# Kernel tuning notes

Hardware: AMD Instinct MI355X
Metric: run time of the kernel (lower is better)

Reference implementation:

```python
import jax, jax.numpy as jnp
import numpy as np

HEADS = 8
DIM_HEAD = 64
SCALE = DIM_HEAD ** -0.5

def layernorm_ch(x, g, eps=1e-5):
    # channel-wise LayerNorm over dim=1 (NCHW), biased variance
    mean = jnp.mean(x, axis=1, keepdims=True)
    var = jnp.var(x, axis=1, keepdims=True)
    return (x - mean) * jax.lax.rsqrt(var + eps) * g[None, :, None, None]

def setup_inputs() -> dict:
    key = jax.random.key(0)
    ks = jax.random.split(key, 4)
    B, C, H, W = 16, 512, 64, 64
    hidden = HEADS * DIM_HEAD
    x = jax.random.normal(ks[0], (B, C, H, W), dtype=jnp.float32)
    w_qkv = jax.random.normal(ks[1], (3 * hidden, C), dtype=jnp.float32) * (C ** -0.5)
    w_out = jax.random.normal(ks[2], (C, hidden), dtype=jnp.float32) * (hidden ** -0.5)
    b_out = jnp.zeros((C,), dtype=jnp.float32)
    g_out = jnp.ones((C,), dtype=jnp.float32)
    g_ln = jnp.ones((C,), dtype=jnp.float32)
    return {"x": x, "w_qkv": w_qkv, "w_out": w_out, "b_out": b_out, "g_out": g_out, "g_ln": g_ln}

def reference(x, w_qkv, w_out, b_out, g_out, g_ln):
    B, C, H, W = x.shape
    n = H * W
    x_norm = layernorm_ch(x, g_ln)
    # 1x1 conv == channel GEMM: [B,3*hidden,H,W]
    qkv = jnp.einsum('oc,bchw->bohw', w_qkv, x_norm)
    q, k, v = jnp.split(qkv, 3, axis=1)
    # b (h d) x y -> b h d n
    def to_heads(t):
        return t.reshape(B, HEADS, DIM_HEAD, n)
    q, k, v = to_heads(q), to_heads(k), to_heads(v)
    q = jax.nn.softmax(q, axis=-2) * SCALE   # softmax over d
    k = jax.nn.softmax(k, axis=-1)           # softmax over n
    v = v / n
    context = jnp.einsum('bhdn,bhen->bhde', k, v)
    out = jnp.einsum('bhde,bhdn->bhen', context, q)
    out = out.reshape(B, HEADS * DIM_HEAD, H, W)
    out = jnp.einsum('oc,bchw->bohw', w_out, out) + b_out[None, :, None, None]
    out = layernorm_ch(out, g_out)
    return out + x
```

## Files before the change

### kernel.cpp

```cpp
#include <hip/hip_runtime.h>
#include <math.h>

#define CCH    512
#define HWN    4096
#define NPIX   65536
#define OC3    1536
#define QSCALE 0.125f
#define LN_EPS 1e-5f

typedef _Float16 h16;
typedef h16  f16x8 __attribute__((ext_vector_type(8)));
typedef h16  f16x4 __attribute__((ext_vector_type(4)));
typedef float f32x4 __attribute__((ext_vector_type(4)));

__device__ __forceinline__ float waveReduceSum(float v) {
#pragma unroll
    for (int off = 32; off; off >>= 1) v += __shfl_xor(v, off);
    return v;
}

__device__ __forceinline__ void gl_lds16(const void* g, void* l) {
    __builtin_amdgcn_global_load_lds((const __attribute__((address_space(1))) void*)g,
                                     (__attribute__((address_space(3))) void*)l, 16, 0, 0);
}

__global__ __launch_bounds__(256) void transpose_prep(const float* __restrict__ src,
                                                      h16* __restrict__ dhi,
                                                      float* __restrict__ psum,
                                                      float* __restrict__ psq,
                                                      const float* __restrict__ w_qkv,
                                                      const float* __restrict__ g_ln,
                                                      const float* __restrict__ w_out,
                                                      h16* __restrict__ wg_h,
                                                      float* __restrict__ s,
                                                      h16* __restrict__ wo_h) {
    __shared__ float tile[64][65];
    __shared__ float ps1[4][64], ps2[4][64];
    const int t = threadIdx.x;

    if (blockIdx.z == 16) {
        const int o = (blockIdx.x + 64 * blockIdx.y) * 4 + (t >> 6);
        const int lane = t & 63;
        if (o < OC3) {
            float sum = 0.f;
#pragma unroll
            for (int j = 0; j < 8; ++j) {
                const int c = lane + j * 64;
                const float w = w_qkv[(size_t)o * CCH + c] * g_ln[c];
                wg_h[(size_t)o * CCH + c] = (h16)(w * 64.f);
                sum += w;
            }
            sum = waveReduceSum(sum);
            if (lane == 0) s[o] = sum;
        } else {
            const int r = o - OC3;
#pragma unroll
            for (int j = 0; j < 8; ++j) {
                const int c = lane + j * 64;
                wo_h[(size_t)r * CCH + c] = (h16)(w_out[(size_t)r * CCH + c] * 64.f);
            }
        }
        return;
    }

    const int b = blockIdx.z, c0 = blockIdx.y * 64, p0 = blockIdx.x * 64;
    const float* sb = src + ((size_t)b * CCH + c0) * HWN + p0;
    const int rc = t >> 4, cc4 = (t & 15) * 4;
#pragma unroll
    for (int ps = 0; ps < 4; ++ps) {
        const float4 v = *(const float4*)(sb + (size_t)(rc + ps * 16) * HWN + cc4);
        tile[rc + ps * 16][cc4 + 0] = v.x;
        tile[rc + ps * 16][cc4 + 1] = v.y;
        tile[rc + ps * 16][cc4 + 2] = v.z;
        tile[rc + ps * 16][cc4 + 3] = v.w;
    }
    __syncthreads();
    {
        const int q = t >> 6, px = t & 63;
        float s1 = 0.f, s2 = 0.f;
#pragma unroll
        for (int c = q * 16; c < q * 16 + 16; ++c) {
            const float v = tile[c][px];
            s1 += v; s2 += v * v;
        }
        ps1[q][px] = s1; ps2[q][px] = s2;
    }
    const int pr0 = t >> 3, cs = (t & 7) * 8;
#pragma unroll
    for (int ps = 0; ps < 2; ++ps) {
        const int pr = pr0 + ps * 32;
        f16x8 vh;
#pragma unroll
        for (int q = 0; q < 8; ++q) vh[q] = (h16)tile[cs + q][pr];
        const size_t o = ((size_t)b * HWN + p0 + pr) * CCH + c0 + cs;
        *(f16x8*)(dhi + o) = vh;
    }
    __syncthreads();
    if (t < 64) {
        const float s1 = ps1[0][t] + ps1[1][t] + ps1[2][t] + ps1[3][t];
        const float s2 = ps2[0][t] + ps2[1][t] + ps2[2][t] + ps2[3][t];
        const size_t gp = (size_t)b * HWN + p0 + t;
        psum[(size_t)(c0 >> 6) * NPIX + gp] = s1;
        psq [(size_t)(c0 >> 6) * NPIX + gp] = s2;
    }
}

__global__ __launch_bounds__(512) void qkv_gemm(const h16* __restrict__ Ahg,
                                                const h16* __restrict__ Bhg,
                                                const float* __restrict__ sv,
                                                const float* __restrict__ psum,
                                                const float* __restrict__ psq,
                                                h16* __restrict__ qout) {
    __shared__ __align__(16) h16 Ah[8192];
    __shared__ __align__(16) h16 Bh[16384];
    __shared__ float mnS[256], rsS[256];
    const int tid = threadIdx.x;
    const int om = blockIdx.x * 128;
    const int by0 = blockIdx.y;
    const int by  = (by0 & 7) * 32 + (by0 >> 3);
    const int p0  = by * 256;

    const int srow = tid >> 2;
    const int skh  = ((tid & 3) ^ (srow & 3)) * 8;
    const size_t a0 = (size_t)(om + srow) * CCH + skh;
    const size_t b0 = (size_t)(p0 + srow) * CCH + skh;

    const int lane = tid & 63;
    const int wv = tid >> 6;
    const int wm = (wv >> 2) * 64, wn = (wv & 3) * 64;
    const int lr = lane & 15, kg = lane >> 4;
    const int swz = (kg ^ (lr & 3)) * 8;

    f32x4 acc[4][4];
#pragma unroll
    for (int i = 0; i < 4; ++i)
#pragma unroll
        for (int j = 0; j < 4; ++j) acc[i][j] = {0.f, 0.f, 0.f, 0.f};

#define STAGE(KC)                                                          \
    do {                                                                   \
        gl_lds16(Ahg + a0 + (KC),                 Ah + tid * 8);           \
        gl_lds16(Ahg + a0 + (KC) + 32,            Ah + 4096 + tid * 8);    \
        gl_lds16(Bhg + b0 + (KC),                 Bh + tid * 8);           \
        gl_lds16(Bhg + b0 + (KC) + 128 * CCH,     Bh + 4096 + tid * 8);    \
        gl_lds16(Bhg + b0 + (KC) + 32,            Bh + 8192 + tid * 8);    \
        gl_lds16(Bhg + b0 + (KC) + 32 + 128 * CCH, Bh + 12288 + tid * 8);  \
    } while (0)

    STAGE(0);
    if (tid < 256) {
        const int gp = p0 + tid;
        float s1 = 0.f, s2 = 0.f;
#pragma unroll
        for (int cb = 0; cb < 8; ++cb) {
            s1 += psum[(size_t)cb * NPIX + gp];
            s2 += psq [(size_t)cb * NPIX + gp];
        }
        const float m = s1 * (1.f / 512.f);
        float var = s2 * (1.f / 512.f) - m * m;
        var = fmaxf(var, 0.f);
        mnS[tid] = m;
        rsS[tid] = rsqrtf(var + LN_EPS);
    }

#pragma unroll 1
    for (int kc = 0; kc < 512; kc += 64) {
        __syncthreads();
        f16x8 a0f[4], b0f[4], a1f[4], b1f[4];
#pragma unroll
        for (int i = 0; i < 4; ++i) {
            a0f[i] = *(const f16x8*)(Ah + (wm + i * 16 + lr) * 32 + swz);
            b0f[i] = *(const f16x8*)(Bh + (wn + i * 16 + lr) * 32 + swz);
        }
#pragma unroll
        for (int i = 0; i < 4; ++i)
#pragma unroll
            for (int j = 0; j < 4; ++j)
                acc[i][j] = __builtin_amdgcn_mfma_f32_16x16x32_f16(a0f[i], b0f[j], acc[i][j], 0, 0, 0);
#pragma unroll
        for (int i = 0; i < 4; ++i) {
            a1f[i] = *(const f16x8*)(Ah + 4096 + (wm + i * 16 + lr) * 32 + swz);
            b1f[i] = *(const f16x8*)(Bh + 8192 + (wn + i * 16 + lr) * 32 + swz);
        }
        __syncthreads();
        if (kc + 64 < 512) STAGE(kc + 64);
#pragma unroll
        for (int i = 0; i < 4; ++i)
#pragma unroll
            for (int j = 0; j < 4; ++j)
                acc[i][j] = __builtin_amdgcn_mfma_f32_16x16x32_f16(a1f[i], b1f[j], acc[i][j], 0, 0, 0);
    }
#undef STAGE

    const int b = p0 >> 12, hw0 = p0 & 4095;
    float mn[4], rs[4];
#pragma unroll
    for (int j = 0; j < 4; ++j) {
        const int px = wn + j * 16 + lr;
        mn[j] = mnS[px]; rs[j] = rsS[px];
    }
#pragma unroll
    for (int i = 0; i < 4; ++i)
#pragma unroll
        for (int r = 0; r < 4; ++r) {
            const int o = om + wm + i * 16 + kg * 4 + r;
            const float so = sv[o];
            h16* dst = qout + ((size_t)b * OC3 + o) * HWN;
#pragma unroll
            for (int j = 0; j < 4; ++j) {
                const int hw = hw0 + wn + j * 16 + lr;
                dst[hw] = (h16)(rs[j] * (acc[i][j][r] * (1.f / 64.f) - mn[j] * so));
            }
        }
}

__global__ __launch_bounds__(64) void ctx_partial(const h16* __restrict__ qkv16,
                                                  float* __restrict__ ctp) {
    const int bh = blockIdx.y, ci = blockIdx.x;
    const int b = bh >> 3, h = bh & 7;
    const h16* kb = qkv16 + ((size_t)b * OC3 + CCH  + h * 64) * HWN;
    const h16* vb = qkv16 + ((size_t)b * OC3 + 1024 + h * 64) * HWN;
    const int lane = threadIdx.x;
    const int lr = lane & 15, kg = lane >> 4;
    const int nbase = ci * 256 + kg * 8;

    float m[4] = {-1e30f, -1e30f, -1e30f, -1e30f};
#pragma unroll 1
    for (int c = 0; c < 8; ++c) {
        const int n0 = nbase + c * 32;
#pragma unroll
        for (int i = 0; i < 4; ++i) {
            const f16x8 kv = *(const f16x8*)(kb + (size_t)(i * 16 + lr) * HWN + n0);
#pragma unroll
            for (int u = 0; u < 8; ++u) m[i] = fmaxf(m[i], (float)kv[u]);
        }
    }
#pragma unroll
    for (int i = 0; i < 4; ++i) {
        m[i] = fmaxf(m[i], __shfl_xor(m[i], 16));
        m[i] = fmaxf(m[i], __shfl_xor(m[i], 32));
    }

    float z[4] = {0.f, 0.f, 0.f, 0.f};
    f32x4 acc[4][4];
#pragma unroll
    for (int i = 0; i < 4; ++i)
#pragma unroll
        for (int j = 0; j < 4; ++j) acc[i][j] = {0.f, 0.f, 0.f, 0.f};

#pragma unroll 1
    for (int c = 0; c < 8; ++c) {
        const int n0 = nbase + c * 32;
        f16x8 ke[4], vf[4];
#pragma unroll
        for (int j = 0; j < 4; ++j)
            vf[j] = *(const f16x8*)(vb + (size_t)(j * 16 + lr) * HWN + n0);
#pragma unroll
        for (int i = 0; i < 4; ++i) {
            const f16x8 kv = *(const f16x8*)(kb + (size_t)(i * 16 + lr) * HWN + n0);
            f16x8 t;
#pragma unroll
            for (int u = 0; u < 8; ++u) {
                const float e = __expf((float)kv[u] - m[i]);
                z[i] += e;
                t[u] = (h16)e;
            }
            ke[i] = t;
        }
#pragma unroll
        for (int i = 0; i < 4; ++i)
#pragma unroll
            for (int j = 0; j < 4; ++j)
                acc[i][j] = __builtin_amdgcn_mfma_f32_16x16x32_f16(ke[i], vf[j], acc[i][j], 0, 0, 0);
    }
#pragma unroll
    for (int i = 0; i < 4; ++i) {
        z[i] += __shfl_xor(z[i], 16);
        z[i] += __shfl_xor(z[i], 32);
    }
    float* dst = ctp + ((size_t)bh * 16 + ci) * 4224;
#pragma unroll
    for (int i = 0; i < 4; ++i)
#pragma unroll
        for (int j = 0; j < 4; ++j)
#pragma unroll
            for (int r = 0; r < 4; ++r)
                dst[(i * 16 + kg * 4 + r) * 64 + j * 16 + lr] = acc[i][j][r];
    if (kg == 0)
#pragma unroll
        for (int i = 0; i < 4; ++i) {
            dst[4096 + i * 16 + lr] = z[i];
            dst[4160 + i * 16 + lr] = m[i];
        }
}

__global__ __launch_bounds__(256) void ctx_reduce(const float* __restrict__ ctp,
                                                  h16* __restrict__ ctt) {
    __shared__ float w[16][64];
    __shared__ float rz[64];
    const int bh = blockIdx.x;
    const int tid = threadIdx.x;
    const float* src = ctp + (size_t)bh * 16 * 4224;
    if (tid < 64) {
        float M = -1e30f;
#pragma unroll
        for (int ci = 0; ci < 16; ++ci)
            M = fmaxf(M, src[(size_t)ci * 4224 + 4160 + tid]);
        float Z = 0.f;
#pragma unroll
        for (int ci = 0; ci < 16; ++ci) {
            const float ww = __expf(src[(size_t)ci * 4224 + 4160 + tid] - M);
            w[ci][tid] = ww;
            Z += ww * src[(size_t)ci * 4224 + 4096 + tid];
        }
        rz[tid] = 1.f / Z;
    }
    __syncthreads();
    h16* dstt = ctt + (size_t)bh * 4096;
    for (int e4 = tid * 4; e4 < 4096; e4 += 1024) {
        const int d = e4 >> 6, e0 = e4 & 63;
        float4 sum = make_float4(0.f, 0.f, 0.f, 0.f);
#pragma unroll
        for (int ci = 0; ci < 16; ++ci) {
            const float4 v = *(const float4*)(src + (size_t)ci * 4224 + e4);
            const float ww = w[ci][d];
            sum.x += ww * v.x; sum.y += ww * v.y;
            sum.z += ww * v.z; sum.w += ww * v.w;
        }
        const float r = rz[d];
        dstt[(e0 + 0) * 64 + d] = (h16)(sum.x * r);
        dstt[(e0 + 1) * 64 + d] = (h16)(sum.y * r);
        dstt[(e0 + 2) * 64 + d] = (h16)(sum.z * r);
        dstt[(e0 + 3) * 64 + d] = (h16)(sum.w * r);
    }
}

__global__ __launch_bounds__(512) void out_fused(const h16* __restrict__ wo_hi,
                                                 const h16* __restrict__ qkv16,
                                                 const h16* __restrict__ ctt,
                                                 const float* __restrict__ b_out,
                                                 const float* __restrict__ g_out,
                                                 const float* __restrict__ x,
                                                 float* __restrict__ out) {
    __shared__ __align__(16) h16 Alds[512 * 32];
    __shared__ __align__(16) h16 qt[128][72];
    __shared__ float red1[4][128], red2[4][128];
    __shared__ float mnS[128], rsS[128];

    const int tid = threadIdx.x;
    const int p0 = blockIdx.x * 128;
    const int b = p0 >> 12, hw0 = p0 & 4095;

    const int trow = tid >> 2;
    const int skh  = ((tid & 3) ^ (trow & 3)) * 8;
    const size_t aoff = (size_t)trow * CCH + skh;
    const int wofs = (tid >> 6) * 512;

    const int wv = tid >> 6;
    const int lane = tid & 63;
    const int lr = lane & 15, kg = lane >> 4;
    const int wm = (wv >> 1) * 128, wn = (wv & 1) * 64;
    const int swz = (kg ^ (lr & 3)) * 8;
    const int pv_e0 = (wv & 3) * 16, pv_ph = (wv >> 2) * 64;
    const int sm_px = tid >> 2, sm_d0 = (tid & 3) * 16;
    const int ql_d = tid >> 3, ql_px = (tid & 7) * 16;

    f32x4 acc[8][4];
#pragma unroll
    for (int i = 0; i < 8; ++i)
#pragma unroll
        for (int j = 0; j < 4; ++j) acc[i][j] = {0.f, 0.f, 0.f, 0.f};

#define STAGEF(S)                                                           \
    do {                                                                    \
        const int kc_ = (S) * 32;                                           \
        gl_lds16(wo_hi + aoff + kc_,               Alds + wofs);            \
        gl_lds16(wo_hi + aoff + kc_ + 128 * CCH,   Alds + 4096 + wofs);     \
        gl_lds16(wo_hi + aoff + kc_ + 256 * CCH,   Alds + 8192 + wofs);     \
        gl_lds16(wo_hi + aoff + kc_ + 384 * CCH,   Alds + 12288 + wofs);    \
    } while (0)

    STAGEF(0);

    f16x8 q0, q1;
    {
        const h16* qb = qkv16 + ((size_t)b * OC3) * HWN + hw0;
        q0 = *(const f16x8*)(qb + (size_t)ql_d * HWN + ql_px);
        q1 = *(const f16x8*)(qb + (size_t)ql_d * HWN + ql_px + 8);
    }

#pragma unroll 1
    for (int h = 0; h < 8; ++h) {
#pragma unroll
        for (int u = 0; u < 8; ++u) {
            qt[ql_px + u][ql_d]     = q0[u];
            qt[ql_px + 8 + u][ql_d] = q1[u];
        }
        __syncthreads();
        {
            float qv[16];
            float mx = -1e30f;
#pragma unroll
            for (int dd = 0; dd < 16; ++dd) {
                qv[dd] = (float)qt[sm_px][sm_d0 + dd];
                mx = fmaxf(mx, qv[dd]);
            }
            mx = fmaxf(mx, __shfl_xor(mx, 1));
            mx = fmaxf(mx, __shfl_xor(mx, 2));
            float sm = 0.f;
#pragma unroll
            for (int dd = 0; dd < 16; ++dd) {
                qv[dd] = __expf(qv[dd] - mx);
                sm += qv[dd];
            }
            sm += __shfl_xor(sm, 1);
            sm += __shfl_xor(sm, 2);
            const float sc = 512.f * QSCALE / sm;
#pragma unroll
            for (int dd = 0; dd < 16; ++dd)
                qt[sm_px][sm_d0 + dd] = (h16)(qv[dd] * sc);
        }
        __syncthreads();
        {
            const h16* cb = ctt + ((size_t)(b * 8 + h)) * 4096 + (pv_e0 + lr) * 64 + kg * 8;
            const f16x8 af0 = *(const f16x8*)(cb);
            const f16x8 af1 = *(const f16x8*)(cb + 32);
            f32x4 acc4[4];
#pragma unroll
            for (int j = 0; j < 4; ++j) acc4[j] = {0.f, 0.f, 0.f, 0.f};
#pragma unroll
            for (int j = 0; j < 4; ++j) {
                const int px = pv_ph + j * 16 + lr;
                const f16x8 bf0 = *(const f16x8*)(&qt[px][kg * 8]);
                const f16x8 bf1 = *(const f16x8*)(&qt[px][32 + kg * 8]);
                acc4[j] = __builtin_amdgcn_mfma_f32_16x16x32_f16(af0, bf0, acc4[j], 0, 0, 0);
                acc4[j] = __builtin_amdgcn_mfma_f32_16x16x32_f16(af1, bf1, acc4[j], 0, 0, 0);
            }
            __syncthreads();
#pragma unroll
            for (int j = 0; j < 4; ++j) {
                f16x4 o4;
                o4[0] = (h16)acc4[j][0]; o4[1] = (h16)acc4[j][1];
                o4[2] = (h16)acc4[j][2]; o4[3] = (h16)acc4[j][3];
                *(f16x4*)(&qt[pv_ph + j * 16 + lr][pv_e0 + kg * 4]) = o4;
            }
        }
        if (h < 7) {
            const h16* qb = qkv16 + ((size_t)b * OC3 + (h + 1) * 64) * HWN + hw0;
            q0 = *(const f16x8*)(qb + (size_t)ql_d * HWN + ql_px);
            q1 = *(const f16x8*)(qb + (size_t)ql_d * HWN + ql_px + 8);
        }
#pragma unroll 1
        for (int ss = 0; ss < 2; ++ss) {
            const int s = 2 * h + ss;
            __syncthreads();
            f16x8 af[8], bf[4];
#pragma unroll
            for (int i = 0; i < 8; ++i)
                af[i] = *(const f16x8*)(Alds + (wm + i * 16 + lr) * 32 + swz);
#pragma unroll
            for (int j = 0; j < 4; ++j)
                bf[j] = *(const f16x8*)(&qt[wn + j * 16 + lr][ss * 32 + kg * 8]);
            __syncthreads();
            if (s < 15) STAGEF(s + 1);
#pragma unroll
            for (int i = 0; i < 8; ++i)
#pragma unroll
                for (int j = 0; j < 4; ++j)
                    acc[i][j] = __builtin_amdgcn_mfma_f32_16x16x32_f16(af[i], bf[j], acc[i][j], 0, 0, 0);
        }
    }
#undef STAGEF

#pragma unroll
    for (int i = 0; i < 8; ++i) {
        const int o = wm + i * 16 + kg * 4;
        const float4 bb = *(const float4*)(b_out + o);
#pragma unroll
        for (int j = 0; j < 4; ++j) {
            acc[i][j][0] = acc[i][j][0] * (1.f / 134217728.f) + bb.x;
            acc[i][j][1] = acc[i][j][1] * (1.f / 134217728.f) + bb.y;
            acc[i][j][2] = acc[i][j][2] * (1.f / 134217728.f) + bb.z;
            acc[i][j][3] = acc[i][j][3] * (1.f / 134217728.f) + bb.w;
        }
    }
    float s1[4], s2[4];
#pragma unroll
    for (int j = 0; j < 4; ++j) {
        s1[j] = 0.f; s2[j] = 0.f;
#pragma unroll
        for (int i = 0; i < 8; ++i)
#pragma unroll
            for (int r = 0; r < 4; ++r) {
                const float v = acc[i][j][r];
                s1[j] += v; s2[j] += v * v;
            }
        s1[j] += __shfl_xor(s1[j], 16); s1[j] += __shfl_xor(s1[j], 32);
        s2[j] += __shfl_xor(s2[j], 16); s2[j] += __shfl_xor(s2[j], 32);
    }
    if (kg == 0) {
#pragma unroll
        for (int j = 0; j < 4; ++j) {
            red1[wv >> 1][wn + j * 16 + lr] = s1[j];
            red2[wv >> 1][wn + j * 16 + lr] = s2[j];
        }
    }
    __syncthreads();
    if (tid < 128) {
        const float S1 = red1[0][tid] + red1[1][tid] + red1[2][tid] + red1[3][tid];
        const float S2 = red2[0][tid] + red2[1][tid] + red2[2][tid] + red2[3][tid];
        const float m = S1 * (1.f / 512.f);
        float var = S2 * (1.f / 512.f) - m * m;
        var = fmaxf(var, 0.f);
        mnS[tid] = m;
        rsS[tid] = rsqrtf(var + LN_EPS);
    }
    __syncthreads();
    float mj[4], rj[4];
#pragma unroll
    for (int j = 0; j < 4; ++j) {
        const int px = wn + j * 16 + lr;
        mj[j] = mnS[px]; rj[j] = rsS[px];
    }
#pragma unroll
    for (int i = 0; i < 8; ++i) {
        const int o = wm + i * 16 + kg * 4;
        const float4 gg = *(const float4*)(g_out + o);
#pragma unroll
        for (int r = 0; r < 4; ++r) {
            const float g = (r == 0) ? gg.x : (r == 1) ? gg.y : (r == 2) ? gg.z : gg.w;
            const float* xr = x + ((size_t)b * CCH + o + r) * HWN + hw0 + wn;
            float* dr = out + ((size_t)b * CCH + o + r) * HWN + hw0 + wn;
#pragma unroll
            for (int j = 0; j < 4; ++j) {
                const int c = j * 16 + lr;
                dr[c] = (acc[i][j][r] - mj[j]) * rj[j] * g + xr[c];
            }
        }
    }
}

extern "C" void kernel_launch(void* const* d_in, const int* in_sizes, int n_in,
                              void* d_out, int out_size, void* d_ws, size_t ws_size,
                              hipStream_t stream) {
    (void)in_sizes; (void)n_in; (void)out_size;
    const float* x     = (const float*)d_in[0];
    const float* w_qkv = (const float*)d_in[1];
    const float* w_out = (const float*)d_in[2];
    const float* b_out = (const float*)d_in[3];
    const float* g_out = (const float*)d_in[4];
    const float* g_ln  = (const float*)d_in[5];
    float* out = (float*)d_out;
    float* ws  = (float*)d_ws;

    float* s    = ws;
    h16*  ctt   = (h16*)(s + OC3);
    float* ctp  = s + OC3 + 524288;
    float* psum = ctp;
    float* psq  = psum + 524288;
    h16*  wg_hi = (h16*)(ctp + 8650752);
    h16*  wo_hi = wg_hi + 786432;
    h16*  qkv16 = wo_hi + 262144;
    h16*  xt_hi = (h16*)d_out;

    const size_t need = 60032512ULL * 4ULL;
    if (ws_size < need) return;

    transpose_prep<<<dim3(64, 8, 17), 256, 0, stream>>>(x, xt_hi, psum, psq,
                                                        w_qkv, g_ln, w_out,
                                                        wg_hi, s, wo_hi);
    qkv_gemm     <<<dim3(12, 256), 512, 0, stream>>>(wg_hi, xt_hi,
                                                     s, psum, psq, qkv16);
    ctx_partial  <<<dim3(16, 128), 64, 0, stream>>>(qkv16, ctp);
    ctx_reduce   <<<128, 256, 0, stream>>>(ctp, ctt);
    out_fused    <<<512, 512, 0, stream>>>(wo_hi, qkv16, ctt,
                                           b_out, g_out, x, out);
}
```

Measured before the change: 378.9 us.

## Triple-buffer QKV GEMM LDS staging with vmcnt-based waits and MFMA priority

Replaces the single-buffer 64-wide K staging in the QKV GEMM with a three-stage ring of 32-wide K slices. Two slices are prefetched ahead and each iteration waits with s_waitcnt vmcnt instead of a full barrier pair, so global-to-LDS loads overlap the MFMA work. It also raises wave priority around the MFMA block and sets launch bounds to one block per CU. The LDS footprint grows and the hand-placed vmcnt counts must match the three loads each stage issues.

```diff
diff --git a/kernel.cpp b/kernel.cpp
--- a/kernel.cpp
+++ b/kernel.cpp
@@ -105,14 +105,13 @@
     }
 }
 
-__global__ __launch_bounds__(512) void qkv_gemm(const h16* __restrict__ Ahg,
-                                                const h16* __restrict__ Bhg,
-                                                const float* __restrict__ sv,
-                                                const float* __restrict__ psum,
-                                                const float* __restrict__ psq,
-                                                h16* __restrict__ qout) {
-    __shared__ __align__(16) h16 Ah[8192];
-    __shared__ __align__(16) h16 Bh[16384];
+__global__ __launch_bounds__(512, 1) void qkv_gemm(const h16* __restrict__ Ahg,
+                                                   const h16* __restrict__ Bhg,
+                                                   const float* __restrict__ sv,
+                                                   const float* __restrict__ psum,
+                                                   const float* __restrict__ psq,
+                                                   h16* __restrict__ qout) {
+    __shared__ __align__(16) h16 lds[36864];
     __shared__ float mnS[256], rsS[256];
     const int tid = threadIdx.x;
     const int om = blockIdx.x * 128;
@@ -137,17 +136,6 @@
 #pragma unroll
         for (int j = 0; j < 4; ++j) acc[i][j] = {0.f, 0.f, 0.f, 0.f};
 
-#define STAGE(KC)                                                          \
-    do {                                                                   \
-        gl_lds16(Ahg + a0 + (KC),                 Ah + tid * 8);           \
-        gl_lds16(Ahg + a0 + (KC) + 32,            Ah + 4096 + tid * 8);    \
-        gl_lds16(Bhg + b0 + (KC),                 Bh + tid * 8);           \
-        gl_lds16(Bhg + b0 + (KC) + 128 * CCH,     Bh + 4096 + tid * 8);    \
-        gl_lds16(Bhg + b0 + (KC) + 32,            Bh + 8192 + tid * 8);    \
-        gl_lds16(Bhg + b0 + (KC) + 32 + 128 * CCH, Bh + 12288 + tid * 8);  \
-    } while (0)
-
-    STAGE(0);
     if (tid < 256) {
         const int gp = p0 + tid;
         float s1 = 0.f, s2 = 0.f;
@@ -162,35 +150,46 @@
         mnS[tid] = m;
         rsS[tid] = rsqrtf(var + LN_EPS);
     }
+    __syncthreads();
+
+#define BUF(k) (lds + (k) * 12288)
+#define STAGE(T)                                                        \
+    do {                                                                \
+        h16* Lb = BUF((T) % 3);                                         \
+        const int kc_ = (T) * 32;                                       \
+        gl_lds16(Ahg + a0 + kc_,             Lb + tid * 8);             \
+        gl_lds16(Bhg + b0 + kc_,             Lb + 4096 + tid * 8);      \
+        gl_lds16(Bhg + b0 + kc_ + 128 * CCH, Lb + 8192 + tid * 8);      \
+    } while (0)
+
+    STAGE(0);
+    STAGE(1);
 
 #pragma unroll 1
-    for (int kc = 0; kc < 512; kc += 64) {
-        __syncthreads();
-        f16x8 a0f[4], b0f[4], a1f[4], b1f[4];
+    for (int t = 0; t < 16; ++t) {
+        if (t == 15) asm volatile("s_waitcnt vmcnt(0)" ::: "memory");
+        else         asm volatile("s_waitcnt vmcnt(3)" ::: "memory");
+        __builtin_amdgcn_sched_barrier(0);
+        __builtin_amdgcn_s_barrier();
+        __builtin_amdgcn_sched_barrier(0);
+        const h16* Rb = BUF(t % 3);
+        f16x8 af[4], bf[4];
 #pragma unroll
         for (int i = 0; i < 4; ++i) {
-            a0f[i] = *(const f16x8*)(Ah + (wm + i * 16 + lr) * 32 + swz);
-            b0f[i] = *(const f16x8*)(Bh + (wn + i * 16 + lr) * 32 + swz);
-        }
+            af[i] = *(const f16x8*)(Rb + (wm + i * 16 + lr) * 32 + swz);
+            bf[i] = *(const f16x8*)(Rb + 4096 + (wn + i * 16 + lr) * 32 + swz);
+        }
+        if (t + 2 < 16) STAGE(t + 2);
+        __builtin_amdgcn_s_setprio(1);
 #pragma unroll
         for (int i = 0; i < 4; ++i)
 #pragma unroll
             for (int j = 0; j < 4; ++j)
-                acc[i][j] = __builtin_amdgcn_mfma_f32_16x16x32_f16(a0f[i], b0f[j], acc[i][j], 0, 0, 0);
-#pragma unroll
-        for (int i = 0; i < 4; ++i) {
-            a1f[i] = *(const f16x8*)(Ah + 4096 + (wm + i * 16 + lr) * 32 + swz);
-            b1f[i] = *(const f16x8*)(Bh + 8192 + (wn + i * 16 + lr) * 32 + swz);
-        }
-        __syncthreads();
-        if (kc + 64 < 512) STAGE(kc + 64);
-#pragma unroll
-        for (int i = 0; i < 4; ++i)
-#pragma unroll
-            for (int j = 0; j < 4; ++j)
-                acc[i][j] = __builtin_amdgcn_mfma_f32_16x16x32_f16(a1f[i], b1f[j], acc[i][j], 0, 0, 0);
+                acc[i][j] = __builtin_amdgcn_mfma_f32_16x16x32_f16(af[i], bf[j], acc[i][j], 0, 0, 0);
+        __builtin_amdgcn_s_setprio(0);
     }
 #undef STAGE
+#undef BUF
 
     const int b = p0 >> 12, hw0 = p0 & 4095;
     float mn[4], rs[4];
```

Result: slower. 390.6 us (+3.1%).
